# Kernel tuning notes

Measured on AMD Instinct MI355X. Metric: run time of the kernel, lower is better.

Reference implementation:

```python
import jax, jax.numpy as jnp
import numpy as np

OUT_F = 8192
IN_F = 8192
RANK = 32
N_TOK = 128


def _pack_ternary(w_q):
    """Pack int8 ternary {-1,0,+1} [out,in] -> uint8 [out,in//4], LSB-first 2-bit codes."""
    enc = (w_q.astype(np.int32) + 1).astype(np.uint8).reshape(w_q.shape[0], -1, 4)
    packed = enc[:, :, 0] | (enc[:, :, 1] << 2) | (enc[:, :, 2] << 4) | (enc[:, :, 3] << 6)
    return packed


def setup_inputs() -> dict:
    key = jax.random.key(0)
    kx, kw, ks, ka, kb, kbias = jax.random.split(key, 6)
    x = jax.random.normal(kx, (N_TOK, IN_F), dtype=jnp.float32)
    # ternary weights in {-1,0,+1}
    w_q = np.asarray(jax.random.randint(kw, (OUT_F, IN_F), -1, 2, dtype=jnp.int32), dtype=np.int8)
    weight_packed = jnp.asarray(_pack_ternary(w_q), dtype=jnp.uint8)
    scale = jax.random.uniform(ks, (OUT_F,), dtype=jnp.float32, minval=0.01, maxval=0.05)
    lora_A = jax.random.normal(ka, (OUT_F, RANK), dtype=jnp.float32) * 0.02
    lora_B = jax.random.normal(kb, (RANK, IN_F), dtype=jnp.float32) * 0.02
    bias = jax.random.normal(kbias, (OUT_F,), dtype=jnp.float32) * 0.01
    return {"x": x, "weight_packed": weight_packed, "scale": scale,
            "lora_A": lora_A, "lora_B": lora_B, "bias": bias, "in_features": IN_F}


def _unpack_ternary(packed, in_features, dtype):
    # packed: uint8 [out, in//4]; LSB-first 2-bit codes, code-1 -> {-1,0,+1}
    p = packed.astype(jnp.int32)
    vals = jnp.stack([p & 3, (p >> 2) & 3, (p >> 4) & 3, (p >> 6) & 3], axis=-1)
    vals = vals.reshape(packed.shape[0], -1)[:, :in_features] - 1
    return vals.astype(dtype)


def reference(x, weight_packed, scale, lora_A, lora_B, bias, in_features):
    W = _unpack_ternary(weight_packed, in_features, x.dtype)  # [out, in]
    out = (x @ W.T) * scale[None, :]                          # [n, out]
    out = out + (x @ lora_B.T) @ lora_A.T                     # low-rank LoRA path
    out = out + bias
    return out
```

## Files before the change

### kernel.cpp

```cpp
#include <hip/hip_runtime.h>
#include <hip/hip_bf16.h>
#include <stdint.h>

typedef float f32x4 __attribute__((ext_vector_type(4)));
typedef __bf16 bf16x8 __attribute__((ext_vector_type(8)));
typedef unsigned short ushort8 __attribute__((ext_vector_type(8)));

typedef const __attribute__((address_space(1))) uint32_t gu32;
typedef __attribute__((address_space(3))) uint32_t lu32;

#define N_TOK 128
#define OUT_F 8192
#define IN_F  8192
#define RANK  32

#define KSPLIT 8
#define KB    (IN_F / KSPLIT)
#define BK    64
#define NSTEP (KB / BK)
#define WSTRIDE 16
#define LKC   4

#define XB_OFF 0
#define TB_OFF ((size_t)N_TOK * IN_F * 2)
#define PO_OFF (TB_OFF + (size_t)LKC * N_TOK * RANK * 4)

__device__ __forceinline__ unsigned short bf16r(float f) {
    uint32_t u = __float_as_uint(f);
    return (unsigned short)((u + 0x7FFFu + ((u >> 16) & 1u)) >> 16);
}

__device__ __forceinline__ int swz(int row, int col) { return col ^ ((row & 7) << 3); }

__global__ __launch_bounds__(256) void cvt_x(const float* __restrict__ x,
                                             unsigned short* __restrict__ xt) {
    size_t f = (size_t)blockIdx.x * 256 + threadIdx.x;
    int c8 = (int)(f & 7);
    int r = (int)((f >> 3) & 127);
    int sblk = (int)(f >> 10);
    int k = sblk * 64 + ((c8 ^ (r & 7)) << 3);
    const float4* sp = (const float4*)(x + (size_t)r * IN_F + k);
    float4 a = sp[0], b = sp[1];
    ushort8 o;
    o[0] = bf16r(a.x); o[1] = bf16r(a.y); o[2] = bf16r(a.z); o[3] = bf16r(a.w);
    o[4] = bf16r(b.x); o[5] = bf16r(b.y); o[6] = bf16r(b.z); o[7] = bf16r(b.w);
    *(ushort8*)(xt + f * 8) = o;
}

__global__ __launch_bounds__(256) void lora_t(const float* __restrict__ x,
                                              const float* __restrict__ lb,
                                              float* __restrict__ tB) {
    __shared__ float ts[256][33];
    __shared__ float ps[8][32];
    const int m = blockIdx.x >> 2, kc = blockIdx.x & 3;
    const int tid = threadIdx.x;
    const int c0 = kc * 2048 + tid * 8;
    float4 xv0 = *(const float4*)(x + (size_t)m * IN_F + c0);
    float4 xv1 = *(const float4*)(x + (size_t)m * IN_F + c0 + 4);
#pragma unroll
    for (int r = 0; r < RANK; ++r) {
        const float4* bp = (const float4*)(lb + (size_t)r * IN_F + c0);
        float4 b0 = bp[0], b1 = bp[1];
        float s = xv0.x * b0.x + xv0.y * b0.y + xv0.z * b0.z + xv0.w * b0.w +
                  xv1.x * b1.x + xv1.y * b1.y + xv1.z * b1.z + xv1.w * b1.w;
        ts[tid][r] = s;
    }
    __syncthreads();
    {
        int g = tid >> 5, r = tid & 31;
        float s = 0.f;
        for (int j = 0; j < 32; ++j) s += ts[g * 32 + j][r];
        ps[g][r] = s;
    }
    __syncthreads();
    if (tid < 32) {
        float s = 0.f;
#pragma unroll
        for (int g = 0; g < 8; ++g) s += ps[g][tid];
        tB[(kc * N_TOK + m) * RANK + tid] = s;
    }
}

__device__ __forceinline__ void decodeW(int4 v, uint32_t d[8]) {
    uint32_t p = (uint32_t)v.x | ((uint32_t)v.y << 8) |
                 ((uint32_t)v.z << 16) | ((uint32_t)v.w << 24);
    const uint32_t HI = 0x403F00BFu;
    const uint32_t LO = 0x00800080u;
#pragma unroll
    for (int j = 0; j < 8; ++j) {
        uint32_t c0 = (p >> (4 * j)) & 3u;
        uint32_t c1 = (p >> (4 * j + 2)) & 3u;
        uint32_t t = c0 | (c1 << 16);
        uint32_t sel = (t | (t << 8)) + 0x04000400u;
        d[j] = __builtin_amdgcn_perm(HI, LO, sel);
    }
}

__global__ __launch_bounds__(256) void ternary_gemm(const unsigned short* __restrict__ xt,
                                                    const int* __restrict__ wp,
                                                    unsigned short* __restrict__ pO) {
    __shared__ unsigned short xs[2][128][64];
    __shared__ unsigned short ww[2][128][64];
    const int tid = threadIdx.x;
    const int nb = blockIdx.x >> 3;
    const int ks = blockIdx.x & 7;
    const int n0 = nb * 128;
    const int lane = tid & 63;
    const int wid = tid >> 6;
    const int wr = wid >> 1, wc = wid & 1;

    const int srow = tid >> 2;
    const int xcol = (tid & 3) * 16;
    const int* pg0 = wp + (size_t)(n0 + srow) * (IN_F / 4) + ks * (KB / 4) + (tid & 3) * 4;
    const int* pg1 = pg0 + (size_t)64 * (IN_F / 4);

    const unsigned short* xsrc = xt + ((size_t)(ks * NSTEP) * 128 + wid * 8) * 64 + lane * 8;

    f32x4 acc[4][4];
#pragma unroll
    for (int i = 0; i < 4; ++i)
#pragma unroll
        for (int j = 0; j < 4; ++j) acc[i][j] = (f32x4){0.f, 0.f, 0.f, 0.f};

    const int arow = lane & 15;
    const int kgrp = (lane >> 4) * 8;
    const int wc0 = swz(srow, xcol), wc1 = swz(srow, xcol + 8);

    int4 wA0 = *(const int4*)(pg0);
    int4 wA1 = *(const int4*)(pg1);
#pragma unroll
    for (int j = 0; j < 4; ++j)
        __builtin_amdgcn_global_load_lds(
            (gu32*)(xsrc + j * 2048),
            (lu32*)((char*)(&xs[0][0][0]) + wid * 1024 + j * 4096), 16, 0, 0);
    int4 wB0 = *(const int4*)(pg0 + WSTRIDE);
    int4 wB1 = *(const int4*)(pg1 + WSTRIDE);
    {
        uint32_t d0[8], d1[8];
        decodeW(wA0, d0);
        decodeW(wA1, d1);
        *(uint4*)&ww[0][srow][wc0]      = make_uint4(d0[0], d0[1], d0[2], d0[3]);
        *(uint4*)&ww[0][srow][wc1]      = make_uint4(d0[4], d0[5], d0[6], d0[7]);
        *(uint4*)&ww[0][srow + 64][wc0] = make_uint4(d1[0], d1[1], d1[2], d1[3]);
        *(uint4*)&ww[0][srow + 64][wc1] = make_uint4(d1[4], d1[5], d1[6], d1[7]);
    }
    __syncthreads();

#pragma unroll
    for (int s = 0; s < NSTEP; ++s) {
        const int cur = s & 1, nxt = cur ^ 1;
        if (s + 2 < NSTEP) {
            if ((s & 1) == 0) {
                wA0 = *(const int4*)(pg0 + (s + 2) * WSTRIDE);
                wA1 = *(const int4*)(pg1 + (s + 2) * WSTRIDE);
            } else {
                wB0 = *(const int4*)(pg0 + (s + 2) * WSTRIDE);
                wB1 = *(const int4*)(pg1 + (s + 2) * WSTRIDE);
            }
        }
        if (s + 1 < NSTEP) {
#pragma unroll
            for (int j = 0; j < 4; ++j)
                __builtin_amdgcn_global_load_lds(
                    (gu32*)(xsrc + (size_t)(s + 1) * (128 * 64) + j * 2048),
                    (lu32*)((char*)(&xs[nxt][0][0]) + wid * 1024 + j * 4096), 16, 0, 0);
            uint32_t d0[8], d1[8];
            if ((s & 1) == 0) { decodeW(wB0, d0); decodeW(wB1, d1); }
            else              { decodeW(wA0, d0); decodeW(wA1, d1); }
            *(uint4*)&ww[nxt][srow][wc0]      = make_uint4(d0[0], d0[1], d0[2], d0[3]);
            *(uint4*)&ww[nxt][srow][wc1]      = make_uint4(d0[4], d0[5], d0[6], d0[7]);
            *(uint4*)&ww[nxt][srow + 64][wc0] = make_uint4(d1[0], d1[1], d1[2], d1[3]);
            *(uint4*)&ww[nxt][srow + 64][wc1] = make_uint4(d1[4], d1[5], d1[6], d1[7]);
        }
#pragma unroll
        for (int kk = 0; kk < 2; ++kk) {
            const int kcol = kk * 32 + kgrp;
            bf16x8 af[4], bfr[4];
#pragma unroll
            for (int ar = 0; ar < 4; ++ar) {
                int row = wr * 64 + ar * 16 + arow;
                af[ar] = *(const bf16x8*)&xs[cur][row][swz(row, kcol)];
            }
#pragma unroll
            for (int br = 0; br < 4; ++br) {
                int row = wc * 64 + br * 16 + arow;
                bfr[br] = *(const bf16x8*)&ww[cur][row][swz(row, kcol)];
            }
#pragma unroll
            for (int ar = 0; ar < 4; ++ar)
#pragma unroll
                for (int br = 0; br < 4; ++br)
                    acc[ar][br] = __builtin_amdgcn_mfma_f32_16x16x32_bf16(
                        af[ar], bfr[br], acc[ar][br], 0, 0, 0);
        }
        __syncthreads();
    }

    unsigned short* po = pO + ((size_t)ks << 20);
    const int mrow = (lane >> 4) * 4;
#pragma unroll
    for (int ar = 0; ar < 4; ++ar) {
#pragma unroll
        for (int br = 0; br < 4; ++br) {
            int m = wr * 64 + ar * 16 + mrow;
            int n = n0 + wc * 64 + br * 16 + arow;
            unsigned short* pp = po + (size_t)m * OUT_F + n;
#pragma unroll
            for (int j = 0; j < 4; ++j) pp[(size_t)j * OUT_F] = bf16r(acc[ar][br][j]);
        }
    }
}

__global__ __launch_bounds__(256) void reduce_out(const unsigned short* __restrict__ pO,
                                                  const float* __restrict__ tB,
                                                  const float* __restrict__ scale,
                                                  const float* __restrict__ lora_A,
                                                  const float* __restrict__ bias,
                                                  float* __restrict__ out) {
    __shared__ float ts[4][RANK];
    int nb = blockIdx.x & 15, mg = blockIdx.x >> 4;
    int tid = threadIdx.x;
    int m0 = mg * 4;
    if (tid < 128) {
        int i = tid >> 5, r = tid & 31;
        float s = 0.f;
#pragma unroll
        for (int c = 0; c < LKC; ++c) s += tB[(c * N_TOK + m0 + i) * RANK + r];
        ts[i][r] = s;
    }
    __syncthreads();
    int n = nb * 512 + tid * 2;
    float sc0 = scale[n], sc1 = scale[n + 1];
    float bs0 = bias[n], bs1 = bias[n + 1];
    float4 a0[8], a1[8];
    const float4* ap0 = (const float4*)(lora_A + (size_t)n * RANK);
    const float4* ap1 = (const float4*)(lora_A + (size_t)(n + 1) * RANK);
#pragma unroll
    for (int q = 0; q < 8; ++q) { a0[q] = ap0[q]; a1[q] = ap1[q]; }
#pragma unroll
    for (int i = 0; i < 4; ++i) {
        int m = m0 + i;
        const unsigned short* pp = pO + (size_t)m * OUT_F + n;
        float s0 = 0.f, s1 = 0.f;
#pragma unroll
        for (int c = 0; c < KSPLIT; ++c) {
            uint32_t u = *(const uint32_t*)(pp + ((size_t)c << 20));
            s0 += __uint_as_float(u << 16);
            s1 += __uint_as_float(u & 0xFFFF0000u);
        }
        float l0 = 0.f, l1 = 0.f;
#pragma unroll
        for (int q = 0; q < 8; ++q) {
            float4 tv = *(const float4*)&ts[i][q * 4];
            l0 = fmaf(tv.x, a0[q].x, l0); l0 = fmaf(tv.y, a0[q].y, l0);
            l0 = fmaf(tv.z, a0[q].z, l0); l0 = fmaf(tv.w, a0[q].w, l0);
            l1 = fmaf(tv.x, a1[q].x, l1); l1 = fmaf(tv.y, a1[q].y, l1);
            l1 = fmaf(tv.z, a1[q].z, l1); l1 = fmaf(tv.w, a1[q].w, l1);
        }
        out[(size_t)m * OUT_F + n]     = fmaf(s0, sc0, l0 + bs0);
        out[(size_t)m * OUT_F + n + 1] = fmaf(s1, sc1, l1 + bs1);
    }
}

extern "C" void kernel_launch(void* const* d_in, const int* in_sizes, int n_in,
                              void* d_out, int out_size, void* d_ws, size_t ws_size,
                              hipStream_t stream) {
    const float* x      = (const float*)d_in[0];
    const int*   wp     = (const int*)d_in[1];
    const float* scale  = (const float*)d_in[2];
    const float* lora_A = (const float*)d_in[3];
    const float* lora_B = (const float*)d_in[4];
    const float* bias   = (const float*)d_in[5];
    float* out = (float*)d_out;

    char* ws = (char*)d_ws;
    unsigned short* xt = (unsigned short*)(ws + XB_OFF);
    float* tB = (float*)(ws + TB_OFF);
    unsigned short* pO = (unsigned short*)(ws + PO_OFF);

    cvt_x<<<512, 256, 0, stream>>>(x, xt);
    lora_t<<<N_TOK * LKC, 256, 0, stream>>>(x, lora_B, tB);
    ternary_gemm<<<(OUT_F / 128) * KSPLIT, 256, 0, stream>>>(xt, wp, pO);
    reduce_out<<<16 * 32, 256, 0, stream>>>(pO, tB, scale, lora_A, bias, out);
}
```

Measured before the change: 54.42 us.

## Decode ternary weights straight into MFMA registers and raise the K split

Removes the LDS staging buffer for decoded weights. Each wave now loads its own packed weight bytes and decodes them in registers straight into MFMA B operands. Wave tiling changes so each wave covers all 128 token rows and 32 output columns, which raises LDS reads of x per wave. The K split doubles to 16 and launch bounds ask for 3 blocks per CU, trading more partial-sum traffic and reduction work for more parallelism and fewer LDS round trips and barriers.

```diff
diff --git a/kernel.cpp b/kernel.cpp
--- a/kernel.cpp
+++ b/kernel.cpp
@@ -5,6 +5,7 @@
 typedef float f32x4 __attribute__((ext_vector_type(4)));
 typedef __bf16 bf16x8 __attribute__((ext_vector_type(8)));
 typedef unsigned short ushort8 __attribute__((ext_vector_type(8)));
+typedef uint32_t u32x4 __attribute__((ext_vector_type(4)));
 
 typedef const __attribute__((address_space(1))) uint32_t gu32;
 typedef __attribute__((address_space(3))) uint32_t lu32;
@@ -14,11 +15,9 @@
 #define IN_F  8192
 #define RANK  32
 
-#define KSPLIT 8
+#define KSPLIT 16
 #define KB    (IN_F / KSPLIT)
-#define BK    64
-#define NSTEP (KB / BK)
-#define WSTRIDE 16
+#define ITERS (KB / 64)
 #define LKC   4
 
 #define XB_OFF 0
@@ -81,129 +80,124 @@
     }
 }
 
-__device__ __forceinline__ void decodeW(int4 v, uint32_t d[8]) {
-    uint32_t p = (uint32_t)v.x | ((uint32_t)v.y << 8) |
-                 ((uint32_t)v.z << 16) | ((uint32_t)v.w << 24);
+__device__ __forceinline__ u32x4 decode8(int2 v) {
+    uint32_t p = (uint32_t)(v.x & 0xFF) | (((uint32_t)(v.y & 0xFF)) << 8);
     const uint32_t HI = 0x403F00BFu;
     const uint32_t LO = 0x00800080u;
-#pragma unroll
-    for (int j = 0; j < 8; ++j) {
+    u32x4 d;
+#pragma unroll
+    for (int j = 0; j < 4; ++j) {
         uint32_t c0 = (p >> (4 * j)) & 3u;
         uint32_t c1 = (p >> (4 * j + 2)) & 3u;
         uint32_t t = c0 | (c1 << 16);
         uint32_t sel = (t | (t << 8)) + 0x04000400u;
         d[j] = __builtin_amdgcn_perm(HI, LO, sel);
     }
-}
-
-__global__ __launch_bounds__(256) void ternary_gemm(const unsigned short* __restrict__ xt,
-                                                    const int* __restrict__ wp,
-                                                    unsigned short* __restrict__ pO) {
+    return d;
+}
+
+__global__ __launch_bounds__(256, 3) void ternary_gemm(const unsigned short* __restrict__ xt,
+                                                       const int* __restrict__ wp,
+                                                       unsigned short* __restrict__ pO) {
     __shared__ unsigned short xs[2][128][64];
-    __shared__ unsigned short ww[2][128][64];
     const int tid = threadIdx.x;
-    const int nb = blockIdx.x >> 3;
-    const int ks = blockIdx.x & 7;
+    const int nb = blockIdx.x >> 4;
+    const int ks = blockIdx.x & 15;
     const int n0 = nb * 128;
     const int lane = tid & 63;
     const int wid = tid >> 6;
-    const int wr = wid >> 1, wc = wid & 1;
-
-    const int srow = tid >> 2;
-    const int xcol = (tid & 3) * 16;
-    const int* pg0 = wp + (size_t)(n0 + srow) * (IN_F / 4) + ks * (KB / 4) + (tid & 3) * 4;
-    const int* pg1 = pg0 + (size_t)64 * (IN_F / 4);
-
-    const unsigned short* xsrc = xt + ((size_t)(ks * NSTEP) * 128 + wid * 8) * 64 + lane * 8;
-
-    f32x4 acc[4][4];
-#pragma unroll
-    for (int i = 0; i < 4; ++i)
-#pragma unroll
-        for (int j = 0; j < 4; ++j) acc[i][j] = (f32x4){0.f, 0.f, 0.f, 0.f};
-
     const int arow = lane & 15;
-    const int kgrp = (lane >> 4) * 8;
-    const int wc0 = swz(srow, xcol), wc1 = swz(srow, xcol + 8);
-
-    int4 wA0 = *(const int4*)(pg0);
-    int4 wA1 = *(const int4*)(pg1);
+    const int kq = lane >> 4;
+
+    const int* pw0 = wp + (size_t)(n0 + wid * 32 + arow) * (IN_F / 4) + ks * (KB / 4) + kq * 2;
+    const int* pw1 = pw0 + (size_t)16 * (IN_F / 4);
+
+    const unsigned short* xsrc = xt + ((size_t)(ks * ITERS) * 128 + wid * 8) * 64 + lane * 8;
+
+    f32x4 acc[8][2];
+#pragma unroll
+    for (int i = 0; i < 8; ++i) { acc[i][0] = (f32x4){0,0,0,0}; acc[i][1] = (f32x4){0,0,0,0}; }
+
 #pragma unroll
     for (int j = 0; j < 4; ++j)
         __builtin_amdgcn_global_load_lds(
             (gu32*)(xsrc + j * 2048),
             (lu32*)((char*)(&xs[0][0][0]) + wid * 1024 + j * 4096), 16, 0, 0);
-    int4 wB0 = *(const int4*)(pg0 + WSTRIDE);
-    int4 wB1 = *(const int4*)(pg1 + WSTRIDE);
-    {
-        uint32_t d0[8], d1[8];
-        decodeW(wA0, d0);
-        decodeW(wA1, d1);
-        *(uint4*)&ww[0][srow][wc0]      = make_uint4(d0[0], d0[1], d0[2], d0[3]);
-        *(uint4*)&ww[0][srow][wc1]      = make_uint4(d0[4], d0[5], d0[6], d0[7]);
-        *(uint4*)&ww[0][srow + 64][wc0] = make_uint4(d1[0], d1[1], d1[2], d1[3]);
-        *(uint4*)&ww[0][srow + 64][wc1] = make_uint4(d1[4], d1[5], d1[6], d1[7]);
-    }
-    __syncthreads();
-
-#pragma unroll
-    for (int s = 0; s < NSTEP; ++s) {
-        const int cur = s & 1, nxt = cur ^ 1;
-        if (s + 2 < NSTEP) {
-            if ((s & 1) == 0) {
-                wA0 = *(const int4*)(pg0 + (s + 2) * WSTRIDE);
-                wA1 = *(const int4*)(pg1 + (s + 2) * WSTRIDE);
-            } else {
-                wB0 = *(const int4*)(pg0 + (s + 2) * WSTRIDE);
-                wB1 = *(const int4*)(pg1 + (s + 2) * WSTRIDE);
-            }
-        }
-        if (s + 1 < NSTEP) {
+    int2 wA0 = *(const int2*)(pw0);
+    int2 wA1 = *(const int2*)(pw0 + 8);
+    int2 wA2 = *(const int2*)(pw1);
+    int2 wA3 = *(const int2*)(pw1 + 8);
+    int2 wB0 = *(const int2*)(pw0 + 16);
+    int2 wB1 = *(const int2*)(pw0 + 24);
+    int2 wB2 = *(const int2*)(pw1 + 16);
+    int2 wB3 = *(const int2*)(pw1 + 24);
+    __syncthreads();
+
+#pragma unroll
+    for (int it = 0; it < ITERS; ++it) {
+        const int cur = it & 1;
+        if (it + 1 < ITERS) {
 #pragma unroll
             for (int j = 0; j < 4; ++j)
                 __builtin_amdgcn_global_load_lds(
-                    (gu32*)(xsrc + (size_t)(s + 1) * (128 * 64) + j * 2048),
-                    (lu32*)((char*)(&xs[nxt][0][0]) + wid * 1024 + j * 4096), 16, 0, 0);
-            uint32_t d0[8], d1[8];
-            if ((s & 1) == 0) { decodeW(wB0, d0); decodeW(wB1, d1); }
-            else              { decodeW(wA0, d0); decodeW(wA1, d1); }
-            *(uint4*)&ww[nxt][srow][wc0]      = make_uint4(d0[0], d0[1], d0[2], d0[3]);
-            *(uint4*)&ww[nxt][srow][wc1]      = make_uint4(d0[4], d0[5], d0[6], d0[7]);
-            *(uint4*)&ww[nxt][srow + 64][wc0] = make_uint4(d1[0], d1[1], d1[2], d1[3]);
-            *(uint4*)&ww[nxt][srow + 64][wc1] = make_uint4(d1[4], d1[5], d1[6], d1[7]);
-        }
-#pragma unroll
-        for (int kk = 0; kk < 2; ++kk) {
-            const int kcol = kk * 32 + kgrp;
-            bf16x8 af[4], bfr[4];
-#pragma unroll
-            for (int ar = 0; ar < 4; ++ar) {
-                int row = wr * 64 + ar * 16 + arow;
-                af[ar] = *(const bf16x8*)&xs[cur][row][swz(row, kcol)];
-            }
-#pragma unroll
-            for (int br = 0; br < 4; ++br) {
-                int row = wc * 64 + br * 16 + arow;
-                bfr[br] = *(const bf16x8*)&ww[cur][row][swz(row, kcol)];
-            }
-#pragma unroll
-            for (int ar = 0; ar < 4; ++ar)
-#pragma unroll
-                for (int br = 0; br < 4; ++br)
-                    acc[ar][br] = __builtin_amdgcn_mfma_f32_16x16x32_bf16(
-                        af[ar], bfr[br], acc[ar][br], 0, 0, 0);
+                    (gu32*)(xsrc + (size_t)(it + 1) * 8192 + j * 2048),
+                    (lu32*)((char*)(&xs[cur ^ 1][0][0]) + wid * 1024 + j * 4096), 16, 0, 0);
+        }
+        u32x4 dk0f0, dk0f1, dk1f0, dk1f1;
+        if ((it & 1) == 0) {
+            dk0f0 = decode8(wA0); dk1f0 = decode8(wA1);
+            dk0f1 = decode8(wA2); dk1f1 = decode8(wA3);
+            if (it + 2 < ITERS) {
+                wA0 = *(const int2*)(pw0 + (it + 2) * 16);
+                wA1 = *(const int2*)(pw0 + (it + 2) * 16 + 8);
+                wA2 = *(const int2*)(pw1 + (it + 2) * 16);
+                wA3 = *(const int2*)(pw1 + (it + 2) * 16 + 8);
+            }
+        } else {
+            dk0f0 = decode8(wB0); dk1f0 = decode8(wB1);
+            dk0f1 = decode8(wB2); dk1f1 = decode8(wB3);
+            if (it + 2 < ITERS) {
+                wB0 = *(const int2*)(pw0 + (it + 2) * 16);
+                wB1 = *(const int2*)(pw0 + (it + 2) * 16 + 8);
+                wB2 = *(const int2*)(pw1 + (it + 2) * 16);
+                wB3 = *(const int2*)(pw1 + (it + 2) * 16 + 8);
+            }
+        }
+        bf16x8 b00 = __builtin_bit_cast(bf16x8, dk0f0);
+        bf16x8 b01 = __builtin_bit_cast(bf16x8, dk0f1);
+        bf16x8 b10 = __builtin_bit_cast(bf16x8, dk1f0);
+        bf16x8 b11 = __builtin_bit_cast(bf16x8, dk1f1);
+        {
+            const int kcol = kq * 8;
+#pragma unroll
+            for (int ar = 0; ar < 8; ++ar) {
+                int row = ar * 16 + arow;
+                bf16x8 af = *(const bf16x8*)&xs[cur][row][swz(row, kcol)];
+                acc[ar][0] = __builtin_amdgcn_mfma_f32_16x16x32_bf16(af, b00, acc[ar][0], 0, 0, 0);
+                acc[ar][1] = __builtin_amdgcn_mfma_f32_16x16x32_bf16(af, b01, acc[ar][1], 0, 0, 0);
+            }
+        }
+        {
+            const int kcol = 32 + kq * 8;
+#pragma unroll
+            for (int ar = 0; ar < 8; ++ar) {
+                int row = ar * 16 + arow;
+                bf16x8 af = *(const bf16x8*)&xs[cur][row][swz(row, kcol)];
+                acc[ar][0] = __builtin_amdgcn_mfma_f32_16x16x32_bf16(af, b10, acc[ar][0], 0, 0, 0);
+                acc[ar][1] = __builtin_amdgcn_mfma_f32_16x16x32_bf16(af, b11, acc[ar][1], 0, 0, 0);
+            }
         }
         __syncthreads();
     }
 
     unsigned short* po = pO + ((size_t)ks << 20);
-    const int mrow = (lane >> 4) * 4;
-#pragma unroll
-    for (int ar = 0; ar < 4; ++ar) {
-#pragma unroll
-        for (int br = 0; br < 4; ++br) {
-            int m = wr * 64 + ar * 16 + mrow;
-            int n = n0 + wc * 64 + br * 16 + arow;
+    const int mrow = kq * 4;
+#pragma unroll
+    for (int ar = 0; ar < 8; ++ar) {
+#pragma unroll
+        for (int br = 0; br < 2; ++br) {
+            int m = ar * 16 + mrow;
+            int n = n0 + wid * 32 + br * 16 + arow;
             unsigned short* pp = po + (size_t)m * OUT_F + n;
 #pragma unroll
             for (int j = 0; j < 4; ++j) pp[(size_t)j * OUT_F] = bf16r(acc[ar][br][j]);
```

Result: slower. 61.31 us (+12.7%).
